# Kernel tuning notes

Measured on AMD Instinct MI355X. Metric: run time of the kernel, lower is better.

The kernel has to match this reference:

```python
import jax, jax.numpy as jnp
import numpy as np

NUM_USERS = 40000
NUM_BUSINESSES = 60000
N = NUM_USERS + NUM_BUSINESSES
HIDDEN = 128
HEADS = 4
E = 200000
BATCH = 4096
NEG_SLOPE = 0.2  # PyG GATConv default


def setup_inputs() -> dict:
    key = jax.random.key(0)
    ks = jax.random.split(key, 20)
    s = 0.05
    inp = {
        "user_table": jax.random.normal(ks[0], (NUM_USERS, HIDDEN), jnp.float32) * s,
        "business_table": jax.random.normal(ks[1], (NUM_BUSINESSES, HIDDEN), jnp.float32) * s,
        # gat1: in=HIDDEN, out=HIDDEN, heads=HEADS
        "W1": jax.random.normal(ks[2], (HIDDEN, HEADS * HIDDEN), jnp.float32) * s,
        "att_src1": jax.random.normal(ks[3], (HEADS, HIDDEN), jnp.float32) * s,
        "att_dst1": jax.random.normal(ks[4], (HEADS, HIDDEN), jnp.float32) * s,
        "b1": jnp.zeros((HEADS * HIDDEN,), jnp.float32),
        # gat2: in=HEADS*HIDDEN, out=HIDDEN, heads=1
        "W2": jax.random.normal(ks[5], (HEADS * HIDDEN, HIDDEN), jnp.float32) * s,
        "att_src2": jax.random.normal(ks[6], (1, HIDDEN), jnp.float32) * s,
        "att_dst2": jax.random.normal(ks[7], (1, HIDDEN), jnp.float32) * s,
        "b2": jnp.zeros((HIDDEN,), jnp.float32),
        # predictor MLP
        "Wp1": jax.random.normal(ks[8], (2 * HIDDEN, HIDDEN), jnp.float32) * s,
        "bp1": jnp.zeros((HIDDEN,), jnp.float32),
        "Wp2": jax.random.normal(ks[9], (HIDDEN, 1), jnp.float32) * s,
        "bp2": jnp.zeros((1,), jnp.float32),
        "user_idx": jax.random.randint(ks[10], (BATCH,), 0, NUM_USERS),
        "business_idx": jax.random.randint(ks[11], (BATCH,), 0, NUM_BUSINESSES) + NUM_USERS,
        "edge_index": jax.random.randint(ks[12], (2, E), 0, N),
    }
    return inp


def gat_conv(x, edge_index, W, att_src, att_dst, bias, heads, out_ch, num_nodes):
    # add self-loops (PyG default add_self_loops=True)
    loop = jnp.arange(num_nodes)
    src = jnp.concatenate([edge_index[0], loop])
    dst = jnp.concatenate([edge_index[1], loop])
    h = (x @ W).reshape(num_nodes, heads, out_ch)            # [N,H,C]
    a_src = jnp.einsum('nhc,hc->nh', h, att_src)             # [N,H]
    a_dst = jnp.einsum('nhc,hc->nh', h, att_dst)             # [N,H]
    e = jax.nn.leaky_relu(a_src[src] + a_dst[dst], NEG_SLOPE)  # [E',H]
    # segment softmax over destination nodes
    emax = jax.ops.segment_max(e, dst, num_segments=num_nodes)
    emax = jnp.where(jnp.isfinite(emax), emax, 0.0)
    ex = jnp.exp(e - emax[dst])
    denom = jax.ops.segment_sum(ex, dst, num_segments=num_nodes)
    alpha = ex / (denom[dst] + 1e-16)                        # [E',H]
    msg = h[src] * alpha[..., None]                          # [E',H,C]
    out = jax.ops.segment_sum(msg, dst, num_segments=num_nodes)  # [N,H,C]
    return out.reshape(num_nodes, heads * out_ch) + bias


def reference(user_table, business_table, W1, att_src1, att_dst1, b1,
              W2, att_src2, att_dst2, b2, Wp1, bp1, Wp2, bp2,
              user_idx, business_idx, edge_index):
    user_emb = user_table[user_idx]                          # [B,HIDDEN]
    business_emb = business_table[business_idx - NUM_USERS]  # [B,HIDDEN]
    x = jnp.zeros((N, HIDDEN), jnp.float32)
    x = x.at[user_idx].set(user_emb)
    x = x.at[business_idx].set(business_emb)
    x = jax.nn.relu(gat_conv(x, edge_index, W1, att_src1, att_dst1, b1, HEADS, HIDDEN, N))
    x = gat_conv(x, edge_index, W2, att_src2, att_dst2, b2, 1, HIDDEN, N)
    feats = jnp.concatenate([x[user_idx], x[business_idx]], axis=1)  # [B,2*HIDDEN]
    hidden = jax.nn.relu(feats @ Wp1 + bp1)
    rating = hidden @ Wp2 + bp2                              # [B,1]
    return rating.squeeze(-1)
```

## Files before the change

### kernel.cpp

```cpp
#include <hip/hip_runtime.h>
#include <cstdint>
#include <cstddef>

#define NU      40000
#define NBZ     60000
#define NN      100000
#define HID     128
#define NHEADS  4
#define NE      200000
#define NBATCH  4096
#define BE      (2 * NBATCH)
#define SMAX    10240
#define CAP     16
#define SLOPE   0.2f

typedef __attribute__((ext_vector_type(8))) short short8v;
typedef __attribute__((ext_vector_type(4))) float f32x4;

__device__ __forceinline__ float lrelu(float x) { return x > 0.f ? x : SLOPE * x; }
__device__ __forceinline__ unsigned short f2bf(float f) {
  unsigned u = __float_as_uint(f);
  u += 0x7FFFu + ((u >> 16) & 1u);
  return (unsigned short)(u >> 16);
}

__global__ void k_init(int* __restrict__ node2slotB, int* __restrict__ flags,
                       int* __restrict__ cnt,
                       const float* __restrict__ W1, const float* __restrict__ W2,
                       const float* __restrict__ Wp1,
                       short* __restrict__ w1t, short* __restrict__ w2t,
                       short* __restrict__ wp1t) {
  int i = blockIdx.x * blockDim.x + threadIdx.x;
  if (i < NN) { node2slotB[i] = -1; flags[i] = 0; }
  if (i < NHEADS * HID * HID) {
    int c = i >> 14, nk = i & 16383, n = nk >> 7, k = nk & 127;
    w1t[i] = (short)f2bf(W1[(size_t)k * 512 + c * 128 + n]);
    w2t[i] = (short)f2bf(W2[(size_t)(c * 128 + k) * 128 + n]);
  }
  if (i < HID * 256) {
    int n = i >> 8, k = i & 255;
    wp1t[i] = (short)f2bf(Wp1[(size_t)k * HID + n]);
  }
  if (i == 0) *cnt = 0;
}

__global__ void k_mark(const int* __restrict__ user_idx, const int* __restrict__ business_idx,
                       int* __restrict__ node2slotB) {
  int i = blockIdx.x * blockDim.x + threadIdx.x;
  if (i >= BE) return;
  int node = (i < NBATCH) ? user_idx[i] : business_idx[i - NBATCH];
  node2slotB[node] = i;
}

#define W1ATT_BLOCKS 64
__global__ __launch_bounds__(256)
void k_frontA(const float* __restrict__ W1,
              const float* __restrict__ att_src1, const float* __restrict__ att_dst1,
              float* __restrict__ wsrc, float* __restrict__ wdst,
              const int* __restrict__ ei, const int* __restrict__ n2sB,
              int* __restrict__ flags) {
  int bid = blockIdx.x, tid = threadIdx.x;
  if (bid >= W1ATT_BLOCKS) {
    int e = (bid - W1ATT_BLOCKS) * 256 + tid;
    if (e < NE) {
      int s = ei[e], d = ei[NE + e];
      if (n2sB[d] >= 0) atomicOr(&flags[s], 2);
      if (n2sB[s] >= 0) atomicOr(&flags[d], 1);
    }
    return;
  }
  __shared__ float red[2][2][8];
  int kk = tid >> 7, c = tid & 127;
  int k = bid * 2 + kk;
  float ps[4], pd[4];
#pragma unroll
  for (int h = 0; h < 4; ++h) {
    float wv = W1[(size_t)k * 512 + h * 128 + c];
    ps[h] = wv * att_src1[h * 128 + c];
    pd[h] = wv * att_dst1[h * 128 + c];
  }
#pragma unroll
  for (int off = 1; off < 64; off <<= 1) {
#pragma unroll
    for (int h = 0; h < 4; ++h) { ps[h] += __shfl_xor(ps[h], off); pd[h] += __shfl_xor(pd[h], off); }
  }
  int half = (tid >> 6) & 1;
  if ((tid & 63) == 0) {
#pragma unroll
    for (int h = 0; h < 4; ++h) { red[kk][half][h] = ps[h]; red[kk][half][h + 4] = pd[h]; }
  }
  __syncthreads();
  if ((tid & 127) == 0) {
#pragma unroll
    for (int h = 0; h < 4; ++h) {
      wsrc[k * 4 + h] = red[kk][0][h] + red[kk][1][h];
      wdst[k * 4 + h] = red[kk][0][h + 4] + red[kk][1][h + 4];
    }
  }
}

#define SCAL1_BLOCKS (BE / 4)
__global__ __launch_bounds__(256)
void k_mid(const float* __restrict__ user_table, const float* __restrict__ business_table,
           const int* __restrict__ user_idx, const int* __restrict__ business_idx,
           const float* __restrict__ wsrc, const float* __restrict__ wdst,
           float* __restrict__ a_src1c, float* __restrict__ a_dst1c,
           const int* __restrict__ n2sB, const int* __restrict__ flags,
           int* __restrict__ slotN, int* __restrict__ slot2node, int* __restrict__ cnt,
           int* __restrict__ fillc1, int* __restrict__ indegS,
           int* __restrict__ fillc2, int* __restrict__ indegB) {
  int bid = blockIdx.x, tid = threadIdx.x;
  if (bid >= SCAL1_BLOCKS) {
    int v = (bid - SCAL1_BLOCKS) * 256 + tid;
    if (v >= NN) return;
    if (v < SMAX) { fillc1[v] = 0; indegS[v] = 0; }
    if (v < BE)   { fillc2[v] = 0; indegB[v] = 0; }
    bool need = (n2sB[v] >= 0) || ((flags[v] & 3) == 3);
    int s = -1;
    if (need) {
      s = atomicAdd(cnt, 1);
      if (s >= SMAX) s = -1;
      else slot2node[s] = v;
    }
    slotN[v] = s;
    return;
  }
  int w = bid * 4 + (tid >> 6);
  int lane = tid & 63;
  int node = (w < NBATCH) ? user_idx[w] : business_idx[w - NBATCH];
  const float* src = (w < NBATCH) ? (user_table + (size_t)node * HID)
                                  : (business_table + (size_t)(node - NU) * HID);
  float2 e = *(const float2*)(src + lane * 2);
  float4 w0s = *(const float4*)(wsrc + (lane * 2) * 4);
  float4 w1s = *(const float4*)(wsrc + (lane * 2 + 1) * 4);
  float4 w0d = *(const float4*)(wdst + (lane * 2) * 4);
  float4 w1d = *(const float4*)(wdst + (lane * 2 + 1) * 4);
  float ss[4] = {e.x * w0s.x + e.y * w1s.x, e.x * w0s.y + e.y * w1s.y,
                 e.x * w0s.z + e.y * w1s.z, e.x * w0s.w + e.y * w1s.w};
  float dd[4] = {e.x * w0d.x + e.y * w1d.x, e.x * w0d.y + e.y * w1d.y,
                 e.x * w0d.z + e.y * w1d.z, e.x * w0d.w + e.y * w1d.w};
#pragma unroll
  for (int off = 1; off < 64; off <<= 1) {
#pragma unroll
    for (int h = 0; h < 4; ++h) { ss[h] += __shfl_xor(ss[h], off); dd[h] += __shfl_xor(dd[h], off); }
  }
  if (lane == 0) {
    float4 o1 = {ss[0], ss[1], ss[2], ss[3]};
    float4 o2 = {dd[0], dd[1], dd[2], dd[3]};
    *(float4*)(a_src1c + w * 4) = o1;
    *(float4*)(a_dst1c + w * 4) = o2;
  }
}

__global__ void k_fillb(const int* __restrict__ ei, const int* __restrict__ n2sB,
                        const int* __restrict__ slotN,
                        int* __restrict__ fillc1, int* __restrict__ indegS, int* __restrict__ list1,
                        int* __restrict__ fillc2, int* __restrict__ indegB, int* __restrict__ list2) {
  int e = blockIdx.x * blockDim.x + threadIdx.x;
  if (e >= NE) return;
  int s = ei[e], d = ei[NE + e];
  int snd = slotN[d];
  if (snd >= 0) {
    atomicAdd(&indegS[snd], 1);
    int sB = n2sB[s];
    if (sB >= 0) { int p = atomicAdd(&fillc1[snd], 1); if (p < CAP) list1[snd * CAP + p] = sB; }
  }
  int dB = n2sB[d];
  if (dB >= 0) {
    atomicAdd(&indegB[dB], 1);
    int sns = slotN[s];
    if (sns >= 0) { int p = atomicAdd(&fillc2[dB], 1); if (p < CAP) list2[dB * CAP + p] = sns; }
  }
}

__global__ __launch_bounds__(256)
void k_agg1emb(const int* __restrict__ slot2node, const int* __restrict__ n2sB,
               const int* __restrict__ indegS, const int* __restrict__ fillc1,
               const int* __restrict__ list1,
               const float* __restrict__ a_src1c, const float* __restrict__ a_dst1c,
               const float* __restrict__ user_table, const float* __restrict__ business_table,
               const int* __restrict__ user_idx, const int* __restrict__ business_idx,
               const int* __restrict__ cntp, short* __restrict__ eaggb) {
  int w = (blockIdx.x * blockDim.x + threadIdx.x) >> 6;
  int lane = threadIdx.x & 63;
  int M = *cntp; if (M > SMAX) M = SMAX;
  if (w >= M) return;
  int v = slot2node[w];
  int dB = n2sB[v];
  float ad[4] = {0.f, 0.f, 0.f, 0.f};
  if (dB >= 0) {
    float4 a = *(const float4*)(a_dst1c + dB * 4);
    ad[0] = a.x; ad[1] = a.y; ad[2] = a.z; ad[3] = a.w;
  }
  int ne = fillc1[w];
  int nnb = indegS[w] + 1 - ne - (dB >= 0 ? 1 : 0);
  float m[4], sum[4], ax[4], ay[4];
#pragma unroll
  for (int h = 0; h < 4; ++h) {
    if (nnb > 0) { m[h] = lrelu(ad[h]); sum[h] = (float)nnb; }
    else { m[h] = -3.0e38f; sum[h] = 0.f; }
    ax[h] = 0.f; ay[h] = 0.f;
  }
  for (int j = (dB >= 0 ? -1 : 0); j < ne; ++j) {
    int sB = (j < 0) ? dB : list1[w * CAP + j];
    float4 as4 = *(const float4*)(a_src1c + sB * 4);
    float as[4] = {as4.x, as4.y, as4.z, as4.w};
    int node = (sB < NBATCH) ? user_idx[sB] : business_idx[sB - NBATCH];
    const float* src = (sB < NBATCH) ? (user_table + (size_t)node * HID)
                                     : (business_table + (size_t)(node - NU) * HID);
    float2 e = *(const float2*)(src + lane * 2);
#pragma unroll
    for (int h = 0; h < 4; ++h) {
      float x = lrelu(as[h] + ad[h]);
      if (x > m[h]) {
        float r = __expf(m[h] - x);
        sum[h] = sum[h] * r + 1.f;
        ax[h] = ax[h] * r + e.x;
        ay[h] = ay[h] * r + e.y;
        m[h] = x;
      } else {
        float p = __expf(x - m[h]);
        sum[h] += p;
        ax[h] += p * e.x;
        ay[h] += p * e.y;
      }
    }
  }
  unsigned short* o = (unsigned short*)eaggb + (size_t)w * 512;
#pragma unroll
  for (int h = 0; h < 4; ++h) {
    float r = 1.f / (sum[h] + 1e-16f);
    unsigned lo = f2bf(ax[h] * r), hi = f2bf(ay[h] * r);
    *(unsigned*)(o + h * 128 + lane * 2) = lo | (hi << 16);
  }
}

__global__ __launch_bounds__(512)
void k_mmf(const short* __restrict__ eaggb, const short* __restrict__ w1t,
           const short* __restrict__ w2t, const float* __restrict__ b1,
           const float* __restrict__ att_src2, const float* __restrict__ att_dst2,
           const int* __restrict__ cntp, float* __restrict__ h2c,
           float* __restrict__ a_src2c, float* __restrict__ a_dst2c) {
  __shared__ unsigned short Tlds[32][520];
  __shared__ float pss[8][32], pdd[8][32];
  int M = *cntp; if (M > SMAX) M = SMAX;
  int row0 = blockIdx.x * 32;
  if (row0 >= M) return;
  int lane = threadIdx.x & 63;
  int w = threadIdx.x >> 6;
  int l15 = lane & 15, g = lane >> 4;
  int kq = g * 8;
  int nnw = w * 16 + l15;
#pragma unroll
  for (int rt = 0; rt < 2; ++rt) {
    int rA = row0 + rt * 16 + l15; if (rA >= M) rA = M - 1;
    const short* ap = eaggb + (size_t)rA * 512 + kq;
#pragma unroll
    for (int c = 0; c < 4; ++c) {
      const short* bp = w1t + ((size_t)c * 128 + nnw) * 128 + kq;
      f32x4 acc = {0.f, 0.f, 0.f, 0.f};
#pragma unroll
      for (int k0 = 0; k0 < 128; k0 += 32) {
        short8v a = *(const short8v*)(ap + c * 128 + k0);
        short8v b = *(const short8v*)(bp + k0);
        acc = __builtin_amdgcn_mfma_f32_16x16x32_bf16(a, b, acc, 0, 0, 0);
      }
      float bv = b1[c * 128 + nnw];
#pragma unroll
      for (int j = 0; j < 4; ++j)
        Tlds[rt * 16 + g * 4 + j][c * 128 + nnw] = f2bf(fmaxf(acc[j] + bv, 0.f));
    }
  }
  __syncthreads();
  float as2 = att_src2[nnw], ad2 = att_dst2[nnw];
#pragma unroll
  for (int rt = 0; rt < 2; ++rt) {
    f32x4 acc = {0.f, 0.f, 0.f, 0.f};
#pragma unroll
    for (int c = 0; c < 4; ++c) {
      const short* bp = w2t + ((size_t)c * 128 + nnw) * 128 + kq;
#pragma unroll
      for (int k0 = 0; k0 < 128; k0 += 32) {
        short8v a = *(const short8v*)&Tlds[rt * 16 + l15][c * 128 + k0 + kq];
        short8v b = *(const short8v*)(bp + k0);
        acc = __builtin_amdgcn_mfma_f32_16x16x32_bf16(a, b, acc, 0, 0, 0);
      }
    }
#pragma unroll
    for (int j = 0; j < 4; ++j) {
      int r = row0 + rt * 16 + g * 4 + j;
      float v = acc[j];
      if (r < M) h2c[(size_t)r * HID + nnw] = v;
      float vs = v * as2, vd = v * ad2;
#pragma unroll
      for (int off = 1; off < 16; off <<= 1) { vs += __shfl_xor(vs, off); vd += __shfl_xor(vd, off); }
      if (l15 == 0) { pss[w][rt * 16 + g * 4 + j] = vs; pdd[w][rt * 16 + g * 4 + j] = vd; }
    }
  }
  __syncthreads();
  int tid = threadIdx.x;
  if (tid < 32 && row0 + tid < M) {
    float ss = 0.f, dd = 0.f;
#pragma unroll
    for (int q = 0; q < 8; ++q) { ss += pss[q][tid]; dd += pdd[q][tid]; }
    a_src2c[row0 + tid] = ss;
    a_dst2c[row0 + tid] = dd;
  }
}

__global__ __launch_bounds__(256)
void k_agg2(const int* __restrict__ user_idx, const int* __restrict__ business_idx,
            const int* __restrict__ n2sB, const int* __restrict__ slotN,
            const int* __restrict__ indegB, const int* __restrict__ fillc2,
            const int* __restrict__ list2,
            const float* __restrict__ a_src2c, const float* __restrict__ a_dst2c,
            const float* __restrict__ h2c, const float* __restrict__ b2,
            short* __restrict__ x2b) {
  int w = (blockIdx.x * blockDim.x + threadIdx.x) >> 6;
  int lane = threadIdx.x & 63;
  if (w >= BE) return;
  int node = (w < NBATCH) ? user_idx[w] : business_idx[w - NBATCH];
  if (n2sB[node] != w) return;
  int snd = slotN[node];
  float ad = a_dst2c[snd];
  int ne = fillc2[w];
  int nnb = indegB[w] - ne;
  float m, sum;
  if (nnb > 0) { m = lrelu(ad); sum = (float)nnb; } else { m = -3.0e38f; sum = 0.f; }
  float a0 = 0.f, a1 = 0.f;
  for (int j = -1; j < ne; ++j) {
    int sn = (j < 0) ? snd : list2[w * CAP + j];
    float x = lrelu(a_src2c[sn] + ad);
    float2 hv = *(const float2*)(h2c + (size_t)sn * HID + lane * 2);
    if (x > m) {
      float r = __expf(m - x);
      sum = sum * r + 1.f;
      a0 = a0 * r + hv.x;
      a1 = a1 * r + hv.y;
      m = x;
    } else {
      float p = __expf(x - m);
      sum += p;
      a0 += p * hv.x;
      a1 += p * hv.y;
    }
  }
  float r = 1.f / (sum + 1e-16f);
  int c0 = lane * 2;
  unsigned lo = f2bf(a0 * r + b2[c0]);
  unsigned hi = f2bf(a1 * r + b2[c0 + 1]);
  *(unsigned*)((unsigned short*)x2b + (size_t)w * HID + c0) = lo | (hi << 16);
}

__global__ __launch_bounds__(512)
void k_mlp(const short* __restrict__ x2b, const short* __restrict__ wp1t,
           const int* __restrict__ user_idx, const int* __restrict__ business_idx,
           const int* __restrict__ n2sB,
           const float* __restrict__ bp1, const float* __restrict__ Wp2,
           const float* __restrict__ bp2, float* __restrict__ out) {
  __shared__ float pout[8][16];
  int row0 = blockIdx.x * 16;
  int lane = threadIdx.x & 63;
  int w = threadIdx.x >> 6;
  int l15 = lane & 15, g = lane >> 4;
  int kq = g * 8;
  int p = row0 + l15;
  int us = n2sB[user_idx[p]];
  int bs = n2sB[business_idx[p]];
  int nn = w * 16 + l15;
  f32x4 acc = {0.f, 0.f, 0.f, 0.f};
  const short* bpw = wp1t + (size_t)nn * 256 + kq;
#pragma unroll
  for (int k0 = 0; k0 < 256; k0 += 32) {
    int slot = (k0 < 128) ? us : bs;
    short8v a = *(const short8v*)(x2b + (size_t)slot * HID + (k0 & 127) + kq);
    short8v b = *(const short8v*)(bpw + k0);
    acc = __builtin_amdgcn_mfma_f32_16x16x32_bf16(a, b, acc, 0, 0, 0);
  }
  float bpv = bp1[nn], wpv = Wp2[nn];
#pragma unroll
  for (int j = 0; j < 4; ++j) {
    float v = fmaxf(acc[j] + bpv, 0.f) * wpv;
#pragma unroll
    for (int off = 1; off < 16; off <<= 1) v += __shfl_xor(v, off);
    if (l15 == 0) pout[w][g * 4 + j] = v;
  }
  __syncthreads();
  int tid = threadIdx.x;
  if (tid < 16) {
    float s = 0.f;
#pragma unroll
    for (int q = 0; q < 8; ++q) s += pout[q][tid];
    out[row0 + tid] = s + bp2[0];
  }
}

extern "C" void kernel_launch(void* const* d_in, const int* in_sizes, int n_in,
                              void* d_out, int out_size, void* d_ws, size_t ws_size,
                              hipStream_t stream) {
  const float* user_table     = (const float*)d_in[0];
  const float* business_table = (const float*)d_in[1];
  const float* W1       = (const float*)d_in[2];
  const float* att_src1 = (const float*)d_in[3];
  const float* att_dst1 = (const float*)d_in[4];
  const float* b1       = (const float*)d_in[5];
  const float* W2       = (const float*)d_in[6];
  const float* att_src2 = (const float*)d_in[7];
  const float* att_dst2 = (const float*)d_in[8];
  const float* b2       = (const float*)d_in[9];
  const float* Wp1      = (const float*)d_in[10];
  const float* bp1      = (const float*)d_in[11];
  const float* Wp2      = (const float*)d_in[12];
  const float* bp2      = (const float*)d_in[13];
  const int* user_idx     = (const int*)d_in[14];
  const int* business_idx = (const int*)d_in[15];
  const int* ei           = (const int*)d_in[16];
  float* out = (float*)d_out;

  char* w = (char*)d_ws;
  size_t used = 0;
  auto alloc = [&](size_t bytes) -> void* {
    void* p = w + used;
    used += (bytes + 255) & ~(size_t)255;
    return p;
  };
  int*   node2slotB = (int*)alloc((size_t)NN * 4);
  int*   flags      = (int*)alloc((size_t)NN * 4);
  int*   slotN      = (int*)alloc((size_t)NN * 4);
  int*   slot2node  = (int*)alloc((size_t)SMAX * 4);
  int*   cnt        = (int*)alloc(256);
  float* wsrc       = (float*)alloc((size_t)HID * 4 * 4);
  float* wdst       = (float*)alloc((size_t)HID * 4 * 4);
  float* a_src1c    = (float*)alloc((size_t)BE * 4 * 4);
  float* a_dst1c    = (float*)alloc((size_t)BE * 4 * 4);
  int*   fillc1     = (int*)alloc((size_t)SMAX * 4);
  int*   indegS     = (int*)alloc((size_t)SMAX * 4);
  int*   list1      = (int*)alloc((size_t)SMAX * CAP * 4);
  int*   fillc2     = (int*)alloc((size_t)BE * 4);
  int*   indegB     = (int*)alloc((size_t)BE * 4);
  int*   list2      = (int*)alloc((size_t)BE * CAP * 4);
  short* w1t        = (short*)alloc((size_t)NHEADS * HID * HID * 2);
  short* w2t        = (short*)alloc((size_t)NHEADS * HID * HID * 2);
  short* wp1t       = (short*)alloc((size_t)HID * 256 * 2);
  short* eaggb      = (short*)alloc((size_t)SMAX * 512 * 2);
  float* h2c        = (float*)alloc((size_t)SMAX * HID * 4);
  float* a_src2c    = (float*)alloc((size_t)SMAX * 4);
  float* a_dst2c    = (float*)alloc((size_t)SMAX * 4);
  short* x2b        = (short*)alloc((size_t)BE * HID * 2);
  if (used > ws_size) return;

  const int T = 256;
  auto cdiv = [](int a, int b) { return (a + b - 1) / b; };

  k_init<<<cdiv(NN, T), T, 0, stream>>>(node2slotB, flags, cnt, W1, W2, Wp1, w1t, w2t, wp1t);
  k_mark<<<cdiv(BE, T), T, 0, stream>>>(user_idx, business_idx, node2slotB);

  k_frontA<<<W1ATT_BLOCKS + cdiv(NE, T), T, 0, stream>>>(
      W1, att_src1, att_dst1, wsrc, wdst, ei, node2slotB, flags);

  k_mid<<<SCAL1_BLOCKS + cdiv(NN, T), T, 0, stream>>>(
      user_table, business_table, user_idx, business_idx, wsrc, wdst,
      a_src1c, a_dst1c, node2slotB, flags, slotN, slot2node, cnt,
      fillc1, indegS, fillc2, indegB);

  k_fillb<<<cdiv(NE, T), T, 0, stream>>>(ei, node2slotB, slotN,
                                         fillc1, indegS, list1, fillc2, indegB, list2);

  k_agg1emb<<<cdiv(SMAX * 64, T), T, 0, stream>>>(
      slot2node, node2slotB, indegS, fillc1, list1, a_src1c, a_dst1c,
      user_table, business_table, user_idx, business_idx, cnt, eaggb);

  k_mmf<<<SMAX / 32, 512, 0, stream>>>(eaggb, w1t, w2t, b1, att_src2, att_dst2,
                                       cnt, h2c, a_src2c, a_dst2c);

  k_agg2<<<cdiv(BE * 64, T), T, 0, stream>>>(user_idx, business_idx, node2slotB, slotN,
                                             indegB, fillc2, list2, a_src2c, a_dst2c,
                                             h2c, b2, x2b);

  k_mlp<<<NBATCH / 16, 512, 0, stream>>>(x2b, wp1t, user_idx, business_idx, node2slotB,
                                         bp1, Wp2, bp2, out);
}
```

Measured before the change: 106.0 us.

## Split fused two-layer GEMM into two 128-row register-tiled MFMA kernels

Replaces the fused k_mmf kernel, which handled 32 rows per block and kept the intermediate in LDS, with two separate kernels. The first computes the per-head W1 GEMM with ReLU into a bf16 global buffer, and the second computes the W2 GEMM plus the attention dot products. Each wave now holds a 4x4 grid of MFMA accumulators over 128-row tiles, which raises operand reuse and cuts repeated weight loads. The cost is an extra launch, a round trip of the intermediate through global memory, and far fewer blocks for the second GEMM (about 80), which may underfill the GPU.

```diff
diff --git a/kernel.cpp b/kernel.cpp
--- a/kernel.cpp
+++ b/kernel.cpp
@@ -235,76 +235,132 @@
   }
 }
 
-__global__ __launch_bounds__(512)
-void k_mmf(const short* __restrict__ eaggb, const short* __restrict__ w1t,
-           const short* __restrict__ w2t, const float* __restrict__ b1,
+__global__ __launch_bounds__(256)
+void k_mm0(const short* __restrict__ A, const short* __restrict__ Bt,
+           const float* __restrict__ bias, const int* __restrict__ cntp,
+           short* __restrict__ T) {
+  int M = *cntp; if (M > SMAX) M = SMAX;
+  int row0 = blockIdx.x * 128;
+  if (row0 >= M) return;
+  int c = blockIdx.y;
+  int lane = threadIdx.x & 63;
+  int wid = threadIdx.x >> 6;
+  int wr = wid >> 1, wc = wid & 1;
+  int l15 = lane & 15, g = lane >> 4;
+  int kq = g * 8;
+  f32x4 acc[4][4];
+#pragma unroll
+  for (int i = 0; i < 4; ++i)
+#pragma unroll
+    for (int j = 0; j < 4; ++j) acc[i][j] = (f32x4){0.f, 0.f, 0.f, 0.f};
+
+  const short* bbase = Bt + ((size_t)c * 128 + wc * 64 + l15) * 128 + kq;
+#pragma unroll
+  for (int k0 = 0; k0 < 128; k0 += 32) {
+    short8v av[4], bv[4];
+#pragma unroll
+    for (int i = 0; i < 4; ++i) {
+      int rA = row0 + wr * 64 + i * 16 + l15; if (rA >= M) rA = M - 1;
+      av[i] = *(const short8v*)(A + (size_t)rA * 512 + c * 128 + k0 + kq);
+    }
+#pragma unroll
+    for (int j = 0; j < 4; ++j)
+      bv[j] = *(const short8v*)(bbase + (size_t)j * 16 * 128 + k0);
+#pragma unroll
+    for (int i = 0; i < 4; ++i)
+#pragma unroll
+      for (int j = 0; j < 4; ++j)
+        acc[i][j] = __builtin_amdgcn_mfma_f32_16x16x32_bf16(av[i], bv[j], acc[i][j], 0, 0, 0);
+  }
+#pragma unroll
+  for (int j = 0; j < 4; ++j) {
+    int col = wc * 64 + j * 16 + l15;
+    float bv = bias[c * 128 + col];
+#pragma unroll
+    for (int i = 0; i < 4; ++i) {
+#pragma unroll
+      for (int q = 0; q < 4; ++q) {
+        int r = row0 + wr * 64 + i * 16 + g * 4 + q;
+        if (r < M)
+          ((unsigned short*)T)[(size_t)r * 512 + c * 128 + col] = f2bf(fmaxf(acc[i][j][q] + bv, 0.f));
+      }
+    }
+  }
+}
+
+__global__ __launch_bounds__(256)
+void k_mm1(const short* __restrict__ T, const short* __restrict__ Bt,
            const float* __restrict__ att_src2, const float* __restrict__ att_dst2,
            const int* __restrict__ cntp, float* __restrict__ h2c,
            float* __restrict__ a_src2c, float* __restrict__ a_dst2c) {
-  __shared__ unsigned short Tlds[32][520];
-  __shared__ float pss[8][32], pdd[8][32];
+  __shared__ float pss[2][128], pdd[2][128];
   int M = *cntp; if (M > SMAX) M = SMAX;
-  int row0 = blockIdx.x * 32;
+  int row0 = blockIdx.x * 128;
   if (row0 >= M) return;
   int lane = threadIdx.x & 63;
-  int w = threadIdx.x >> 6;
+  int wid = threadIdx.x >> 6;
+  int wr = wid >> 1, wc = wid & 1;
   int l15 = lane & 15, g = lane >> 4;
   int kq = g * 8;
-  int nnw = w * 16 + l15;
-#pragma unroll
-  for (int rt = 0; rt < 2; ++rt) {
-    int rA = row0 + rt * 16 + l15; if (rA >= M) rA = M - 1;
-    const short* ap = eaggb + (size_t)rA * 512 + kq;
-#pragma unroll
-    for (int c = 0; c < 4; ++c) {
-      const short* bp = w1t + ((size_t)c * 128 + nnw) * 128 + kq;
-      f32x4 acc = {0.f, 0.f, 0.f, 0.f};
-#pragma unroll
-      for (int k0 = 0; k0 < 128; k0 += 32) {
-        short8v a = *(const short8v*)(ap + c * 128 + k0);
-        short8v b = *(const short8v*)(bp + k0);
-        acc = __builtin_amdgcn_mfma_f32_16x16x32_bf16(a, b, acc, 0, 0, 0);
+  f32x4 acc[4][4];
+#pragma unroll
+  for (int i = 0; i < 4; ++i)
+#pragma unroll
+    for (int j = 0; j < 4; ++j) acc[i][j] = (f32x4){0.f, 0.f, 0.f, 0.f};
+
+#pragma unroll
+  for (int ks = 0; ks < 16; ++ks) {
+    int kk = ks * 32;
+    int c = kk >> 7, kc = kk & 127;
+    short8v av[4], bv[4];
+#pragma unroll
+    for (int i = 0; i < 4; ++i) {
+      int rA = row0 + wr * 64 + i * 16 + l15; if (rA >= M) rA = M - 1;
+      av[i] = *(const short8v*)(T + (size_t)rA * 512 + kk + kq);
+    }
+#pragma unroll
+    for (int j = 0; j < 4; ++j)
+      bv[j] = *(const short8v*)(Bt + ((size_t)c * 128 + wc * 64 + j * 16 + l15) * 128 + kc + kq);
+#pragma unroll
+    for (int i = 0; i < 4; ++i)
+#pragma unroll
+      for (int j = 0; j < 4; ++j)
+        acc[i][j] = __builtin_amdgcn_mfma_f32_16x16x32_bf16(av[i], bv[j], acc[i][j], 0, 0, 0);
+  }
+  float as2[4], ad2[4];
+#pragma unroll
+  for (int j = 0; j < 4; ++j) {
+    int col = wc * 64 + j * 16 + l15;
+    as2[j] = att_src2[col];
+    ad2[j] = att_dst2[col];
+  }
+#pragma unroll
+  for (int i = 0; i < 4; ++i) {
+#pragma unroll
+    for (int q = 0; q < 4; ++q) {
+      int r = row0 + wr * 64 + i * 16 + g * 4 + q;
+      float vs = 0.f, vd = 0.f;
+#pragma unroll
+      for (int j = 0; j < 4; ++j) {
+        float v = acc[i][j][q];
+        if (r < M) h2c[(size_t)r * HID + wc * 64 + j * 16 + l15] = v;
+        vs += v * as2[j];
+        vd += v * ad2[j];
       }
-      float bv = b1[c * 128 + nnw];
-#pragma unroll
-      for (int j = 0; j < 4; ++j)
-        Tlds[rt * 16 + g * 4 + j][c * 128 + nnw] = f2bf(fmaxf(acc[j] + bv, 0.f));
-    }
-  }
-  __syncthreads();
-  float as2 = att_src2[nnw], ad2 = att_dst2[nnw];
-#pragma unroll
-  for (int rt = 0; rt < 2; ++rt) {
-    f32x4 acc = {0.f, 0.f, 0.f, 0.f};
-#pragma unroll
-    for (int c = 0; c < 4; ++c) {
-      const short* bp = w2t + ((size_t)c * 128 + nnw) * 128 + kq;
-#pragma unroll
-      for (int k0 = 0; k0 < 128; k0 += 32) {
-        short8v a = *(const short8v*)&Tlds[rt * 16 + l15][c * 128 + k0 + kq];
-        short8v b = *(const short8v*)(bp + k0);
-        acc = __builtin_amdgcn_mfma_f32_16x16x32_bf16(a, b, acc, 0, 0, 0);
+#pragma unroll
+      for (int off = 1; off < 16; off <<= 1) { vs += __shfl_xor(vs, off); vd += __shfl_xor(vd, off); }
+      if (l15 == 0) {
+        int rl = wr * 64 + i * 16 + g * 4 + q;
+        pss[wc][rl] = vs;
+        pdd[wc][rl] = vd;
       }
-    }
-#pragma unroll
-    for (int j = 0; j < 4; ++j) {
-      int r = row0 + rt * 16 + g * 4 + j;
-      float v = acc[j];
-      if (r < M) h2c[(size_t)r * HID + nnw] = v;
-      float vs = v * as2, vd = v * ad2;
-#pragma unroll
-      for (int off = 1; off < 16; off <<= 1) { vs += __shfl_xor(vs, off); vd += __shfl_xor(vd, off); }
-      if (l15 == 0) { pss[w][rt * 16 + g * 4 + j] = vs; pdd[w][rt * 16 + g * 4 + j] = vd; }
     }
   }
   __syncthreads();
   int tid = threadIdx.x;
-  if (tid < 32 && row0 + tid < M) {
-    float ss = 0.f, dd = 0.f;
-#pragma unroll
-    for (int q = 0; q < 8; ++q) { ss += pss[q][tid]; dd += pdd[q][tid]; }
-    a_src2c[row0 + tid] = ss;
-    a_dst2c[row0 + tid] = dd;
+  if (tid < 128 && row0 + tid < M) {
+    a_src2c[row0 + tid] = pss[0][tid] + pss[1][tid];
+    a_dst2c[row0 + tid] = pdd[0][tid] + pdd[1][tid];
   }
 }
 
@@ -443,6 +499,7 @@
   short* w2t        = (short*)alloc((size_t)NHEADS * HID * HID * 2);
   short* wp1t       = (short*)alloc((size_t)HID * 256 * 2);
   short* eaggb      = (short*)alloc((size_t)SMAX * 512 * 2);
+  short* tbufb      = (short*)alloc((size_t)SMAX * 512 * 2);
   float* h2c        = (float*)alloc((size_t)SMAX * HID * 4);
   float* a_src2c    = (float*)alloc((size_t)SMAX * 4);
   float* a_dst2c    = (float*)alloc((size_t)SMAX * 4);
@@ -470,8 +527,9 @@
       slot2node, node2slotB, indegS, fillc1, list1, a_src1c, a_dst1c,
       user_table, business_table, user_idx, business_idx, cnt, eaggb);
 
-  k_mmf<<<SMAX / 32, 512, 0, stream>>>(eaggb, w1t, w2t, b1, att_src2, att_dst2,
-                                       cnt, h2c, a_src2c, a_dst2c);
+  k_mm0<<<dim3(SMAX / 128, NHEADS), T, 0, stream>>>(eaggb, w1t, b1, cnt, tbufb);
+  k_mm1<<<dim3(SMAX / 128, 1), T, 0, stream>>>(tbufb, w2t, att_src2, att_dst2,
+                                               cnt, h2c, a_src2c, a_dst2c);
 
   k_agg2<<<cdiv(BE * 64, T), T, 0, stream>>>(user_idx, business_idx, node2slotB, slotN,
                                              indegB, fillc2, list2, a_src2c, a_dst2c,
```

Measured after the change: 111.0 us. 1.05x slower.
